# Performance work log

Measured on AMD Instinct MI355X. Metric: run time of the kernel, lower is better.

## Reference

```python
import jax, jax.numpy as jnp
import numpy as np

K = 3            # opt.kernel_size
L = 2            # opt.map_layers
MARGIN = 0.1     # opt.global_margin
NEG_NUM = 3      # opt.neg_num
FIRST_PAD = (K - 1) * L // 2


def conv2d(x, w, pad):
    return jax.lax.conv_general_dilated(x, w, (1, 1), [(pad, pad), (pad, pad)],
                                        dimension_numbers=('NCHW', 'OIHW', 'NCHW'))


def mask2weight(m, pad):
    ker = jnp.ones((1, 1, K, K), jnp.float32)
    w = conv2d(m.astype(jnp.float32)[None, None], ker, pad)[0, 0]
    return jnp.where(w > 0, 1.0 / jnp.maximum(w, 1.0), 0.0)


def setup_inputs():
    key = jax.random.key(0)
    ks = jax.random.split(key, 10)
    b, c, d, t, Lw = 8, 128, 64, 64, 20
    P = d * t
    v_map = jax.random.normal(ks[0], (b, c, d, t), jnp.float32)
    words = jax.random.normal(ks[1], (b, Lw, c), jnp.float32)
    w_masks = jnp.ones((b, Lw), jnp.float32)
    v_mask = jnp.triu(jnp.ones((d, t), jnp.float32))
    valid_num = jax.random.randint(ks[2], (b,), d // 2, t + 1)
    iou_maps = jax.random.uniform(ks[3], (P, P), jnp.float32)
    lam = jnp.float32(0.5)
    sc = np.float32(1.0 / np.sqrt(c * K * K))
    sp = np.float32(1.0 / np.sqrt(c))
    Wc0 = jax.random.normal(ks[4], (c, c, K, K), jnp.float32) * sc
    Wc1 = jax.random.normal(ks[5], (c, c, K, K), jnp.float32) * sc
    bc0 = jnp.zeros((c,), jnp.float32)
    bc1 = jnp.zeros((c,), jnp.float32)
    Wp0 = jax.random.normal(ks[6], (c, c), jnp.float32) * sp
    bp0 = jnp.zeros((c,), jnp.float32)
    Wp1 = jax.random.normal(ks[7], (c, c), jnp.float32) * sp
    bp1 = jnp.zeros((c,), jnp.float32)
    W2d = jax.random.normal(ks[8], (1, c, 1, 1), jnp.float32) * sp
    b2d = jnp.zeros((1,), jnp.float32)
    return dict(v_map=v_map, words=words, w_masks=w_masks, v_mask=v_mask,
                valid_num=valid_num, iou_maps=iou_maps, lam=lam,
                Wc0=Wc0, bc0=bc0, Wc1=Wc1, bc1=bc1,
                Wp0=Wp0, bp0=bp0, Wp1=Wp1, bp1=bp1, W2d=W2d, b2d=b2d)


def _forward(v_map, words, w_masks, v_mask, valid_num, iou_maps, lam,
             Wc0, bc0, Wc1, bc1, Wp0, bp0, Wp1, bp1, W2d, b2d):
    b, c, d, t = v_map.shape
    P = d * t
    neg_inf = jnp.float32(-jnp.inf)
    # mask-normalized conv weights, recomputed from v_mask as in __init__
    weight0 = mask2weight(v_mask, FIRST_PAD)          # [d+2*FIRST_PAD-K+1, ...]
    weight1 = mask2weight(weight0 > 0, 0)             # back to [d, t]
    cols = jnp.arange(t)
    vm3 = (v_mask[None] > 0) & (cols[None, None, :] < valid_num[:, None, None])  # [b,d,t]

    def per_sentence(i):
        wm = w_masks[i]
        pooled = (words[i] * wm[:, None]).sum(0) / jnp.maximum(wm.sum(), 1.0)  # [c]
        g0 = jnp.tanh(pooled @ Wp0 + bp0)
        g1 = jnp.tanh(pooled @ Wp1 + bp1)
        # layer 1 (padded), layer 2 (unpadded) -- word-gated, mask-normalized convs
        x = conv2d(v_map, Wc0, FIRST_PAD) + bc0[None, :, None, None]
        x = jax.nn.relu(x * weight0[None, None] * g0[None, :, None, None])
        x = conv2d(x, Wc1, 0) + bc1[None, :, None, None]
        x = jax.nn.relu(x * weight1[None, None] * g1[None, :, None, None])
        s = jax.nn.sigmoid(conv2d(x, W2d, 0)[:, 0] + b2d[0])  # [b, d, t]
        s = jnp.where(vm3, s, neg_inf)
        pmap_i = s[i]
        sflat = s.reshape(b, P)
        pos = sflat.max(1)          # per-video score for sentence i -> [b]
        si = sflat[i]
        pos_idx = jnp.argmax(si)
        iou_row = iou_maps[pos_idx]  # IoU of best proposal vs all proposals
        negs = jnp.where((iou_row < lam) & jnp.isfinite(si), si, neg_inf)
        hard = negs.max()           # hardest NMS-suppressed negative proposal
        neg_loss = jax.nn.relu(MARGIN + hard - pos[i])
        return pos, pmap_i, neg_loss

    scores, positive_map, neg_losses = jax.lax.map(per_sentence, jnp.arange(b))
    negative_loss = neg_losses.mean()
    diagonal = jnp.diag(scores)[:, None]
    cost_s = jax.nn.relu(MARGIN + scores - diagonal)      # sentence -> video
    cost_im = jax.nn.relu(MARGIN + scores - diagonal.T)   # video -> sentence
    eye = jnp.eye(b, dtype=bool)
    cost_s = jnp.where(eye, 0.0, cost_s)
    cost_im = jnp.where(eye, 0.0, cost_im)
    # max_violation: keep NEG_NUM hardest negatives (sort desc == top_k)
    cost_s = jax.lax.top_k(cost_s, NEG_NUM)[0]
    cost_im = jax.lax.top_k(cost_im.T, NEG_NUM)[0]
    loss = cost_s.sum() / b + cost_im.sum() / b + negative_loss
    return loss, positive_map


def reference(v_map, words, w_masks, v_mask, valid_num, iou_maps, lam,
              Wc0, bc0, Wc1, bc1, Wp0, bp0, Wp1, bp1, W2d, b2d):
    return _forward(v_map, words, w_masks, v_mask, valid_num, iou_maps, lam,
                    Wc0, bc0, Wc1, bc1, Wp0, bp0, Wp1, bp1, W2d, b2d)
```

## Files before the change

kernel.cpp:

```cpp
#include <hip/hip_runtime.h>
#include <hip/hip_bf16.h>
#include <math.h>

#define BB 8
#define CC 128
#define DD 64
#define TT 64
#define PP 4096
#define H1 66
#define LW 20
#define MARGINF 0.1f
#define NEG_SENTINEL -1.0e30f

#define Y0_OFF   0
#define VT_OFF   2230272
#define BP0_OFF  4327424
#define NL_OFF   4401152
#define W0_OFF   4479236
#define W1_OFF   4483592
#define G0_OFF   4487688
#define G1_OFF   4488712
#define S_OFF    4489736
#define SCP_OFF  4522504
#define BP1S_OFF 4522632

typedef __attribute__((ext_vector_type(8))) short bf16x8;
typedef __attribute__((ext_vector_type(4))) float f32x4;

#define ASTR 44

__device__ __forceinline__ unsigned f2bf(float f) {
  union { float f; unsigned u; } v; v.f = f;
  unsigned r = v.u + 0x7fffu + ((v.u >> 16) & 1u);
  return r >> 16;
}
__device__ __forceinline__ float bf2f(unsigned hw) {
  union { unsigned u; float f; } v; v.u = hw << 16;
  return v.f;
}
__device__ __forceinline__ unsigned cvt_bf(float x) {
  __hip_bfloat16 h = __float2bfloat16(x);
  union { __hip_bfloat16 h; unsigned short u; } cv; cv.h = h;
  return (unsigned)cv.u;
}

__device__ __forceinline__ unsigned selbf(unsigned d, unsigned W) {
  unsigned diff = (d ^ W) & 0x80008000u;
  unsigned full = (diff >> 15) * 0xFFFFu;
  return d & ~full;
}

__global__ __launch_bounds__(256) void gates_kernel(
    const float* __restrict__ words, const float* __restrict__ w_masks,
    const float* __restrict__ Wp0, const float* __restrict__ bp0,
    const float* __restrict__ Wp1, const float* __restrict__ bp1,
    float* __restrict__ ws)
{
  __shared__ float smem[CC];
  int i = blockIdx.x;
  int t = threadIdx.x;
  if (t < CC) {
    float wsum = 0.f, acc = 0.f;
    for (int l = 0; l < LW; ++l) {
      float wm = w_masks[i * LW + l];
      wsum += wm;
      acc += words[(i * LW + l) * CC + t] * wm;
    }
    smem[t] = acc / fmaxf(wsum, 1.f);
  }
  __syncthreads();
  {
    int c = t & 127;
    const float* Wp = (t < 128) ? Wp0 : Wp1;
    const float* bp = (t < 128) ? bp0 : bp1;
    float a = bp[c];
    for (int k = 0; k < CC; ++k) a += smem[k] * Wp[k * CC + c];
    float g = tanhf(a);
    float* gout = ws + ((t < 128) ? G0_OFF : G1_OFF);
    gout[i * CC + c] = g;
  }
}

__global__ __launch_bounds__(256) void setup_kernel(
    const float* __restrict__ vmap, const float* __restrict__ v_mask,
    const float* __restrict__ Wc0, const float* __restrict__ Wc1,
    float* __restrict__ ws)
{
  __shared__ float smem[64 * 129];
  int bid = blockIdx.x;
  int t = threadIdx.x;

  if (bid < 576) {
    unsigned short* dst = (unsigned short*)(ws + BP0_OFF);
    int idx = bid * 256 + t;
    int j    = idx & 7;
    int lane = (idx >> 3) & 63;
    int cog  = (idx >> 9) & 7;
    int cic  = (idx >> 12) & 3;
    int kk   = idx >> 14;
    int co = cog * 16 + (lane & 15);
    int ci = cic * 32 + (lane >> 4) * 8 + j;
    dst[idx] = (unsigned short)f2bf(Wc0[(co * CC + ci) * 9 + kk]);
  } else if (bid < 1152) {
    for (int v = t; v < 8 * CC; v += 256) smem[v] = ws[G0_OFF + v];
    __syncthreads();
    int idx = (bid - 576) * 256 + t;
    int j    = idx & 7;
    int lane = (idx >> 3) & 63;
    int cog  = (idx >> 9) & 7;
    int cic  = (idx >> 12) & 3;
    int kk   = idx >> 14;
    int co = cog * 16 + (lane & 15);
    int ci = cic * 32 + (lane >> 4) * 8 + j;
    float wv = Wc1[(co * CC + ci) * 9 + kk];
    unsigned short* dst = (unsigned short*)(ws + BP1S_OFF);
#pragma unroll
    for (int si = 0; si < 8; ++si)
      dst[si * 147456 + idx] = (unsigned short)f2bf(wv * smem[si * CC + ci]);
  } else if (bid < 1664) {
    unsigned short* vT = (unsigned short*)(ws + VT_OFF);
    int b = bid - 1152;
    int n = b & 7, y = b >> 3;
    int x = t & 63, c4 = t >> 6;
    for (int rep = 0; rep < 32; ++rep) {
      int ci = rep * 4 + c4;
      smem[x * 129 + ci] = vmap[(((size_t)n * CC + ci) * DD + y) * TT + x];
    }
    __syncthreads();
    for (int rep = 0; rep < 16; ++rep) {
      int v = t + rep * 256;
      int xx = v >> 6, cip = v & 63;
      float a = smem[xx * 129 + cip * 2];
      float b2 = smem[xx * 129 + cip * 2 + 1];
      unsigned pk = f2bf(a) | (f2bf(b2) << 16);
      *(unsigned*)&vT[(((size_t)(n * DD + y) * TT + xx)) * CC + cip * 2] = pk;
    }
  } else {
    if (t < 128) ((unsigned*)(ws + SCP_OFF))[t] = 0u;
    float* w0 = ws + W0_OFF;
    float* w1 = ws + W1_OFF;
    for (int idx = t; idx < H1 * H1; idx += 256) {
      int y = idx / H1, x = idx % H1;
      float cnt = 0.f;
      for (int ky = 0; ky < 3; ++ky)
        for (int kx = 0; kx < 3; ++kx) {
          int iy = y + ky - 2, ix = x + kx - 2;
          if (iy >= 0 && iy < DD && ix >= 0 && ix < TT) cnt += v_mask[iy * TT + ix];
        }
      w0[idx] = (cnt > 0.f) ? 1.f / fmaxf(cnt, 1.f) : 0.f;
    }
    __syncthreads();
    for (int idx = t; idx < DD * TT; idx += 256) {
      int y = idx / TT, x = idx % TT;
      float cnt = 0.f;
      for (int ky = 0; ky < 3; ++ky)
        for (int kx = 0; kx < 3; ++kx)
          cnt += (w0[(y + ky) * H1 + (x + kx)] > 0.f) ? 1.f : 0.f;
      w1[idx] = (cnt > 0.f) ? 1.f / fmaxf(cnt, 1.f) : 0.f;
    }
  }
}

__global__ __launch_bounds__(256, 2) void conv1_mfma(
    const float* __restrict__ bc0, float* __restrict__ ws)
{
  const unsigned short* vT = (const unsigned short*)(ws + VT_OFF);
  const unsigned short* Bp = (const unsigned short*)(ws + BP0_OFF);
  const float* w0arr = ws + W0_OFF;
  unsigned short* y0w = (unsigned short*)(ws + Y0_OFF);

  __shared__ unsigned short Alds[3 * 68 * ASTR];

  int t = threadIdx.x;
  int id = blockIdx.x + 66 * blockIdx.y;
  int n  = id & 7;
  int r0 = id >> 3;
  int lane = t & 63, w = t >> 6;
  int l15 = lane & 15, l4 = lane >> 4;
  int co0 = w * 32;

  f32x4 acc[5][2];
#pragma unroll
  for (int mf = 0; mf < 5; ++mf)
#pragma unroll
    for (int nf = 0; nf < 2; ++nf) acc[mf][nf] = (f32x4){0.f, 0.f, 0.f, 0.f};

  for (int cic = 0; cic < 4; ++cic) {
    __syncthreads();
    for (int u = t; u < 816; u += 256) {
      int cig = u & 3, rest = u >> 2;
      int col = rest % 68, r = rest / 68;
      int iy = r0 - 2 + r, ix = col - 2;
      uint4 val = {0u, 0u, 0u, 0u};
      if (iy >= 0 && iy < DD && ix >= 0 && ix < TT)
        val = *(const uint4*)&vT[(((size_t)(n * DD + iy) * TT + ix)) * CC + cic * 32 + cig * 8];
      *(uint4*)&Alds[(r * 68 + col) * ASTR + cig * 8] = val;
    }
    __syncthreads();
    __builtin_amdgcn_s_setprio(1);
#pragma unroll
    for (int kk = 0; kk < 9; ++kk) {
      int ky = kk / 3, kx = kk % 3;
      bf16x8 af[5], bfr[2];
#pragma unroll
      for (int mf = 0; mf < 5; ++mf) {
        int c = mf * 16 + l15;
        int cc = c > 65 ? 65 : c;
        af[mf] = *(const bf16x8*)&Alds[(ky * 68 + cc + kx) * ASTR + l4 * 8];
      }
#pragma unroll
      for (int nf = 0; nf < 2; ++nf)
        bfr[nf] = *(const bf16x8*)&Bp[(((kk * 4 + cic) * 8 + w * 2 + nf) * 64 + lane) * 8];
#pragma unroll
      for (int mf = 0; mf < 5; ++mf)
#pragma unroll
        for (int nf = 0; nf < 2; ++nf)
          acc[mf][nf] = __builtin_amdgcn_mfma_f32_16x16x32_bf16(af[mf], bfr[nf], acc[mf][nf], 0, 0, 0);
    }
    __builtin_amdgcn_s_setprio(0);
  }

  int y = r0;
#pragma unroll
  for (int nf = 0; nf < 2; ++nf) {
    int co = co0 + nf * 16 + l15;
    float bcv = bc0[co];
#pragma unroll
    for (int mf = 0; mf < 5; ++mf)
#pragma unroll
      for (int rg = 0; rg < 4; ++rg) {
        int c = mf * 16 + l4 * 4 + rg;
        if (c < H1) {
          float v = (acc[mf][nf][rg] + bcv) * w0arr[y * H1 + c];
          y0w[((size_t)(n * H1 + y) * H1 + c) * CC + co] = (unsigned short)cvt_bf(v);
        }
      }
  }
}

__global__ __launch_bounds__(256, 3) void conv2_mfma(
    const float* __restrict__ bc1, const float* __restrict__ W2d,
    const float* __restrict__ b2d, const float* __restrict__ v_mask,
    const int* __restrict__ valid_num, float* __restrict__ ws,
    float* __restrict__ out)
{
  const unsigned short* y0w = (const unsigned short*)(ws + Y0_OFF);
  const float* w1m = ws + W1_OFF;
  const float* g0 = ws + G0_OFF;
  const float* g1 = ws + G1_OFF;
  unsigned long long* scp = (unsigned long long*)(ws + SCP_OFF);

  __shared__ unsigned short Alds[4 * 66 * ASTR];
  __shared__ unsigned msk[16][4];
  __shared__ float redl[2][2][64];
  __shared__ unsigned long long kred[2];

  int t = threadIdx.x;
  int r0 = blockIdx.x;
  int i = blockIdx.y & 7, n = blockIdx.y >> 3;
  int lane = t & 63, w = t >> 6;
  int wr = w >> 1, wc = w & 1;
  int l15 = lane & 15, l4 = lane >> 4;

  const unsigned short* Bp = (const unsigned short*)(ws + BP1S_OFF) + (size_t)i * 147456;

  if (t < 16) {
    int ch = t * 8;
    msk[t][0] = (g0[i * CC + ch + 0] > 0.f ? 0u : 0x8000u) | (g0[i * CC + ch + 1] > 0.f ? 0u : 0x80000000u);
    msk[t][1] = (g0[i * CC + ch + 2] > 0.f ? 0u : 0x8000u) | (g0[i * CC + ch + 3] > 0.f ? 0u : 0x80000000u);
    msk[t][2] = (g0[i * CC + ch + 4] > 0.f ? 0u : 0x8000u) | (g0[i * CC + ch + 5] > 0.f ? 0u : 0x80000000u);
    msk[t][3] = (g0[i * CC + ch + 6] > 0.f ? 0u : 0x8000u) | (g0[i * CC + ch + 7] > 0.f ? 0u : 0x80000000u);
  }

  f32x4 acc[4][4];
#pragma unroll
  for (int mf = 0; mf < 4; ++mf)
#pragma unroll
    for (int nf = 0; nf < 4; ++nf) acc[mf][nf] = (f32x4){0.f, 0.f, 0.f, 0.f};

  for (int cic = 0; cic < 4; ++cic) {
    __syncthreads();
    {
      uint4 mv = *(const uint4*)&msk[(cic << 2) | (t & 3)][0];
      for (int u = t; u < 1056; u += 256) {
        int cig = u & 3, cr = u >> 2;
        int col = cr % 66, row = cr / 66;
        const unsigned short* src = y0w
            + ((size_t)((n * H1 + r0 * 2 + row) * H1 + col)) * CC + cic * 32 + cig * 8;
        uint4 raw = *(const uint4*)src;
        uint4 pk;
        pk.x = selbf(raw.x, mv.x);
        pk.y = selbf(raw.y, mv.y);
        pk.z = selbf(raw.z, mv.z);
        pk.w = selbf(raw.w, mv.w);
        *(uint4*)&Alds[(row * 66 + col) * ASTR + cig * 8] = pk;
      }
    }
    __syncthreads();
    __builtin_amdgcn_s_setprio(1);
#pragma unroll
    for (int kk = 0; kk < 9; ++kk) {
      int ky = kk / 3, kx = kk % 3;
      bf16x8 af[4], bfr[4];
#pragma unroll
      for (int mf = 0; mf < 4; ++mf) {
        int row = wr + ky;
        int col = mf * 16 + l15 + kx;
        af[mf] = *(const bf16x8*)&Alds[(row * 66 + col) * ASTR + l4 * 8];
      }
#pragma unroll
      for (int nf = 0; nf < 4; ++nf)
        bfr[nf] = *(const bf16x8*)&Bp[(((kk * 4 + cic) * 8 + wc * 4 + nf) * 64 + lane) * 8];
#pragma unroll
      for (int mf = 0; mf < 4; ++mf)
#pragma unroll
        for (int nf = 0; nf < 4; ++nf)
          acc[mf][nf] = __builtin_amdgcn_mfma_f32_16x16x32_bf16(af[mf], bfr[nf], acc[mf][nf], 0, 0, 0);
    }
    __builtin_amdgcn_s_setprio(0);
  }

  float part[4][4];
#pragma unroll
  for (int mf = 0; mf < 4; ++mf)
#pragma unroll
    for (int rg = 0; rg < 4; ++rg) part[mf][rg] = 0.f;
#pragma unroll
  for (int nf = 0; nf < 4; ++nf) {
    int co = wc * 64 + nf * 16 + l15;
    float bcv = bc1[co];
    float gv = g1[i * CC + co];
    float wv = W2d[co];
#pragma unroll
    for (int mf = 0; mf < 4; ++mf)
#pragma unroll
      for (int rg = 0; rg < 4; ++rg) {
        float z = (acc[mf][nf][rg] + bcv) * gv;
        part[mf][rg] += fmaxf(z, 0.f) * wv;
      }
  }
#pragma unroll
  for (int mask = 1; mask < 16; mask <<= 1)
#pragma unroll
    for (int mf = 0; mf < 4; ++mf)
#pragma unroll
      for (int rg = 0; rg < 4; ++rg)
        part[mf][rg] += __shfl_xor(part[mf][rg], mask, 64);
  if (l15 == 0) {
#pragma unroll
    for (int mf = 0; mf < 4; ++mf)
#pragma unroll
      for (int rg = 0; rg < 4; ++rg)
        redl[wc][wr][mf * 16 + l4 * 4 + rg] = part[mf][rg];
  }
  __syncthreads();
  if (t < 128) {
    int row = t >> 6, col = t & 63;
    int rowg = r0 * 2 + row;
    float v = redl[0][row][col] + redl[1][row][col];
    float logit = w1m[rowg * TT + col] * v + b2d[0];
    float sig = 1.f / (1.f + expf(-logit));
    bool m = (v_mask[rowg * TT + col] > 0.f) && (col < valid_num[n]);
    int p = rowg * TT + col;
    if (i == n) {
      ws[S_OFF + i * PP + p] = m ? sig : -INFINITY;
      out[1 + i * PP + p] = m ? sig : NEG_SENTINEL;
    }
    unsigned long long key = 0ull;
    if (m) key = ((unsigned long long)__float_as_uint(sig) << 32)
                 | (unsigned long long)(0xFFFFFFFFu - (unsigned)p);
#pragma unroll
    for (int mk = 1; mk < 64; mk <<= 1) {
      unsigned lo = __shfl_xor((unsigned)key, mk, 64);
      unsigned hi = __shfl_xor((unsigned)(key >> 32), mk, 64);
      unsigned long long o = ((unsigned long long)hi << 32) | lo;
      if (o > key) key = o;
    }
    if (lane == 0) kred[w] = key;
  }
  __syncthreads();
  if (t == 0) {
    unsigned long long k = kred[0];
    if (kred[1] > k) k = kred[1];
    if (k) atomicMax(&scp[i * 8 + n], k);
  }
}

__global__ __launch_bounds__(256) void mine_kernel(
    const float* __restrict__ iou_maps, const float* __restrict__ lam,
    float* __restrict__ ws)
{
  __shared__ float wred[4];
  int i = blockIdx.x;
  int t = threadIdx.x, lane = t & 63, w = t >> 6;
  const unsigned long long* scp = (const unsigned long long*)(ws + SCP_OFF);

  unsigned long long dk = scp[i * 9];
  float diag_sc = __uint_as_float((unsigned)(dk >> 32));
  int pidx = (int)(0xFFFFFFFFu - (unsigned)(dk & 0xFFFFFFFFu));
  float lamv = lam[0];
  const float* row = iou_maps + (size_t)pidx * PP;
  const float* si = ws + S_OFF + (size_t)i * PP;
  float hv = -INFINITY;
  for (int p = t; p < PP; p += 256) {
    float v = si[p];
    if (row[p] < lamv && isfinite(v)) hv = fmaxf(hv, v);
  }
#pragma unroll
  for (int m = 1; m < 64; m <<= 1) hv = fmaxf(hv, __shfl_xor(hv, m, 64));
  if (lane == 0) wred[w] = hv;
  __syncthreads();
  if (t == 0) {
    float h = fmaxf(fmaxf(wred[0], wred[1]), fmaxf(wred[2], wred[3]));
    ws[NL_OFF + i] = fmaxf(0.f, MARGINF + h - diag_sc);
  }
}

__global__ __launch_bounds__(64) void loss_kernel(
    float* __restrict__ ws, float* __restrict__ out)
{
  __shared__ float scsh[64];
  int lane = threadIdx.x;
  const unsigned long long* scp = (const unsigned long long*)(ws + SCP_OFF);
  scsh[lane] = __uint_as_float((unsigned)(scp[lane] >> 32));
  __syncthreads();

  float partial = 0.f;
  if (lane < 16) {
    int r = lane & 7;
    bool im = lane >= 8;
    float diag = scsh[r * 8 + r];
    float v[8];
#pragma unroll
    for (int j = 0; j < 8; ++j) {
      float scv = im ? scsh[j * 8 + r] : scsh[r * 8 + j];
      float h = fmaxf(0.f, MARGINF + scv - diag);
      v[j] = (j == r) ? 0.f : h;
    }
#define CE(a, b) { float mx = fmaxf(v[a], v[b]); float mn = fminf(v[a], v[b]); v[a] = mx; v[b] = mn; }
    CE(0,1) CE(2,3) CE(4,5) CE(6,7)
    CE(0,2) CE(1,3) CE(4,6) CE(5,7)
    CE(1,2) CE(5,6)
    CE(0,4) CE(1,5) CE(2,6) CE(3,7)
    CE(2,4) CE(3,5)
    CE(1,2) CE(3,4) CE(5,6)
#undef CE
    partial = v[0] + v[1] + v[2];
  } else if (lane >= 16 && lane < 24) {
    partial = ws[NL_OFF + lane - 16];
  }
#pragma unroll
  for (int m = 1; m < 64; m <<= 1) partial += __shfl_xor(partial, m, 64);
  if (lane == 0) out[0] = partial * 0.125f;
}

extern "C" void kernel_launch(void* const* d_in, const int* in_sizes, int n_in,
                              void* d_out, int out_size, void* d_ws, size_t ws_size,
                              hipStream_t stream)
{
  const float* v_map     = (const float*)d_in[0];
  const float* words     = (const float*)d_in[1];
  const float* w_masks   = (const float*)d_in[2];
  const float* v_mask    = (const float*)d_in[3];
  const int*   valid_num = (const int*)d_in[4];
  const float* iou_maps  = (const float*)d_in[5];
  const float* lam       = (const float*)d_in[6];
  const float* Wc0 = (const float*)d_in[7];
  const float* bc0 = (const float*)d_in[8];
  const float* Wc1 = (const float*)d_in[9];
  const float* bc1 = (const float*)d_in[10];
  const float* Wp0 = (const float*)d_in[11];
  const float* bp0 = (const float*)d_in[12];
  const float* Wp1 = (const float*)d_in[13];
  const float* bp1 = (const float*)d_in[14];
  const float* W2d = (const float*)d_in[15];
  const float* b2d = (const float*)d_in[16];
  float* ws  = (float*)d_ws;
  float* out = (float*)d_out;

  hipLaunchKernelGGL(gates_kernel, dim3(8), dim3(256), 0, stream,
                     words, w_masks, Wp0, bp0, Wp1, bp1, ws);
  hipLaunchKernelGGL(setup_kernel, dim3(1665), dim3(256), 0, stream,
                     v_map, v_mask, Wc0, Wc1, ws);
  hipLaunchKernelGGL(conv1_mfma, dim3(66, 8), dim3(256), 0, stream, bc0, ws);
  hipLaunchKernelGGL(conv2_mfma, dim3(32, 64), dim3(256), 0, stream,
                     bc1, W2d, b2d, v_mask, valid_num, ws, out);
  hipLaunchKernelGGL(mine_kernel, dim3(8), dim3(256), 0, stream, iou_maps, lam, ws);
  hipLaunchKernelGGL(loss_kernel, dim3(1), dim3(64), 0, stream, ws, out);
}
```

Before: 141.8 us.

## Fuse gates into setup, move Wc1 prep into conv1, split conv1 channels

```diff
diff --git a/kernel.cpp b/kernel.cpp
--- a/kernel.cpp
+++ b/kernel.cpp
@@ -50,40 +50,12 @@
   return d & ~full;
 }
 
-__global__ __launch_bounds__(256) void gates_kernel(
+__global__ __launch_bounds__(256) void setup_kernel(
+    const float* __restrict__ vmap, const float* __restrict__ v_mask,
+    const float* __restrict__ Wc0,
     const float* __restrict__ words, const float* __restrict__ w_masks,
     const float* __restrict__ Wp0, const float* __restrict__ bp0,
     const float* __restrict__ Wp1, const float* __restrict__ bp1,
-    float* __restrict__ ws)
-{
-  __shared__ float smem[CC];
-  int i = blockIdx.x;
-  int t = threadIdx.x;
-  if (t < CC) {
-    float wsum = 0.f, acc = 0.f;
-    for (int l = 0; l < LW; ++l) {
-      float wm = w_masks[i * LW + l];
-      wsum += wm;
-      acc += words[(i * LW + l) * CC + t] * wm;
-    }
-    smem[t] = acc / fmaxf(wsum, 1.f);
-  }
-  __syncthreads();
-  {
-    int c = t & 127;
-    const float* Wp = (t < 128) ? Wp0 : Wp1;
-    const float* bp = (t < 128) ? bp0 : bp1;
-    float a = bp[c];
-    for (int k = 0; k < CC; ++k) a += smem[k] * Wp[k * CC + c];
-    float g = tanhf(a);
-    float* gout = ws + ((t < 128) ? G0_OFF : G1_OFF);
-    gout[i * CC + c] = g;
-  }
-}
-
-__global__ __launch_bounds__(256) void setup_kernel(
-    const float* __restrict__ vmap, const float* __restrict__ v_mask,
-    const float* __restrict__ Wc0, const float* __restrict__ Wc1,
     float* __restrict__ ws)
 {
   __shared__ float smem[64 * 129];
@@ -101,25 +73,9 @@
     int co = cog * 16 + (lane & 15);
     int ci = cic * 32 + (lane >> 4) * 8 + j;
     dst[idx] = (unsigned short)f2bf(Wc0[(co * CC + ci) * 9 + kk]);
-  } else if (bid < 1152) {
-    for (int v = t; v < 8 * CC; v += 256) smem[v] = ws[G0_OFF + v];
-    __syncthreads();
-    int idx = (bid - 576) * 256 + t;
-    int j    = idx & 7;
-    int lane = (idx >> 3) & 63;
-    int cog  = (idx >> 9) & 7;
-    int cic  = (idx >> 12) & 3;
-    int kk   = idx >> 14;
-    int co = cog * 16 + (lane & 15);
-    int ci = cic * 32 + (lane >> 4) * 8 + j;
-    float wv = Wc1[(co * CC + ci) * 9 + kk];
-    unsigned short* dst = (unsigned short*)(ws + BP1S_OFF);
-#pragma unroll
-    for (int si = 0; si < 8; ++si)
-      dst[si * 147456 + idx] = (unsigned short)f2bf(wv * smem[si * CC + ci]);
-  } else if (bid < 1664) {
+  } else if (bid < 1088) {
     unsigned short* vT = (unsigned short*)(ws + VT_OFF);
-    int b = bid - 1152;
+    int b = bid - 576;
     int n = b & 7, y = b >> 3;
     int x = t & 63, c4 = t >> 6;
     for (int rep = 0; rep < 32; ++rep) {
@@ -135,7 +91,7 @@
       unsigned pk = f2bf(a) | (f2bf(b2) << 16);
       *(unsigned*)&vT[(((size_t)(n * DD + y) * TT + xx)) * CC + cip * 2] = pk;
     }
-  } else {
+  } else if (bid == 1088) {
     if (t < 128) ((unsigned*)(ws + SCP_OFF))[t] = 0u;
     float* w0 = ws + W0_OFF;
     float* w1 = ws + W1_OFF;
@@ -158,32 +114,76 @@
           cnt += (w0[(y + ky) * H1 + (x + kx)] > 0.f) ? 1.f : 0.f;
       w1[idx] = (cnt > 0.f) ? 1.f / fmaxf(cnt, 1.f) : 0.f;
     }
-  }
-}
-
-__global__ __launch_bounds__(256, 2) void conv1_mfma(
-    const float* __restrict__ bc0, float* __restrict__ ws)
-{
+  } else {
+    int i = bid - 1089;
+    if (t < CC) {
+      float wsum = 0.f, acc = 0.f;
+      for (int l = 0; l < LW; ++l) {
+        float wm = w_masks[i * LW + l];
+        wsum += wm;
+        acc += words[(i * LW + l) * CC + t] * wm;
+      }
+      smem[t] = acc / fmaxf(wsum, 1.f);
+    }
+    __syncthreads();
+    {
+      int c = t & 127;
+      const float* Wp = (t < 128) ? Wp0 : Wp1;
+      const float* bp = (t < 128) ? bp0 : bp1;
+      float a = bp[c];
+      for (int k = 0; k < CC; ++k) a += smem[k] * Wp[k * CC + c];
+      float g = tanhf(a);
+      float* gout = ws + ((t < 128) ? G0_OFF : G1_OFF);
+      gout[i * CC + c] = g;
+    }
+  }
+}
+
+__global__ __launch_bounds__(256, 3) void conv1_mfma(
+    const float* __restrict__ bc0, const float* __restrict__ Wc1,
+    float* __restrict__ ws)
+{
+  __shared__ unsigned short Alds[3 * 68 * ASTR];
+
+  int t = threadIdx.x;
+  int id = blockIdx.x;
+
+  if (id >= 1056) {
+    float* smem = (float*)Alds;
+    for (int v = t; v < 8 * CC; v += 256) smem[v] = ws[G0_OFF + v];
+    __syncthreads();
+    int idx = (id - 1056) * 256 + t;
+    int j    = idx & 7;
+    int lane = (idx >> 3) & 63;
+    int cog  = (idx >> 9) & 7;
+    int cic  = (idx >> 12) & 3;
+    int kk   = idx >> 14;
+    int co = cog * 16 + (lane & 15);
+    int ci = cic * 32 + (lane >> 4) * 8 + j;
+    float wv = Wc1[(co * CC + ci) * 9 + kk];
+    unsigned short* dst = (unsigned short*)(ws + BP1S_OFF);
+#pragma unroll
+    for (int si = 0; si < 8; ++si)
+      dst[si * 147456 + idx] = (unsigned short)f2bf(wv * smem[si * CC + ci]);
+    return;
+  }
+
   const unsigned short* vT = (const unsigned short*)(ws + VT_OFF);
   const unsigned short* Bp = (const unsigned short*)(ws + BP0_OFF);
   const float* w0arr = ws + W0_OFF;
   unsigned short* y0w = (unsigned short*)(ws + Y0_OFF);
 
-  __shared__ unsigned short Alds[3 * 68 * ASTR];
-
-  int t = threadIdx.x;
-  int id = blockIdx.x + 66 * blockIdx.y;
   int n  = id & 7;
-  int r0 = id >> 3;
+  int ch = (id >> 3) & 1;
+  int r0 = id >> 4;
   int lane = t & 63, w = t >> 6;
   int l15 = lane & 15, l4 = lane >> 4;
-  int co0 = w * 32;
-
-  f32x4 acc[5][2];
-#pragma unroll
-  for (int mf = 0; mf < 5; ++mf)
-#pragma unroll
-    for (int nf = 0; nf < 2; ++nf) acc[mf][nf] = (f32x4){0.f, 0.f, 0.f, 0.f};
+  int s = ch * 4 + w;
+  int co0 = s * 16;
+
+  f32x4 acc[5];
+#pragma unroll
+  for (int mf = 0; mf < 5; ++mf) acc[mf] = (f32x4){0.f, 0.f, 0.f, 0.f};
 
   for (int cic = 0; cic < 4; ++cic) {
     __syncthreads();
@@ -201,29 +201,24 @@
 #pragma unroll
     for (int kk = 0; kk < 9; ++kk) {
       int ky = kk / 3, kx = kk % 3;
-      bf16x8 af[5], bfr[2];
+      bf16x8 af[5], bfr;
 #pragma unroll
       for (int mf = 0; mf < 5; ++mf) {
         int c = mf * 16 + l15;
         int cc = c > 65 ? 65 : c;
         af[mf] = *(const bf16x8*)&Alds[(ky * 68 + cc + kx) * ASTR + l4 * 8];
       }
-#pragma unroll
-      for (int nf = 0; nf < 2; ++nf)
-        bfr[nf] = *(const bf16x8*)&Bp[(((kk * 4 + cic) * 8 + w * 2 + nf) * 64 + lane) * 8];
+      bfr = *(const bf16x8*)&Bp[(((kk * 4 + cic) * 8 + s) * 64 + lane) * 8];
 #pragma unroll
       for (int mf = 0; mf < 5; ++mf)
-#pragma unroll
-        for (int nf = 0; nf < 2; ++nf)
-          acc[mf][nf] = __builtin_amdgcn_mfma_f32_16x16x32_bf16(af[mf], bfr[nf], acc[mf][nf], 0, 0, 0);
+        acc[mf] = __builtin_amdgcn_mfma_f32_16x16x32_bf16(af[mf], bfr, acc[mf], 0, 0, 0);
     }
     __builtin_amdgcn_s_setprio(0);
   }
 
   int y = r0;
-#pragma unroll
-  for (int nf = 0; nf < 2; ++nf) {
-    int co = co0 + nf * 16 + l15;
+  {
+    int co = co0 + l15;
     float bcv = bc0[co];
 #pragma unroll
     for (int mf = 0; mf < 5; ++mf)
@@ -231,7 +226,7 @@
       for (int rg = 0; rg < 4; ++rg) {
         int c = mf * 16 + l4 * 4 + rg;
         if (c < H1) {
-          float v = (acc[mf][nf][rg] + bcv) * w0arr[y * H1 + c];
+          float v = (acc[mf][rg] + bcv) * w0arr[y * H1 + c];
           y0w[((size_t)(n * H1 + y) * H1 + c) * CC + co] = (unsigned short)cvt_bf(v);
         }
       }
@@ -478,11 +473,9 @@
   float* ws  = (float*)d_ws;
   float* out = (float*)d_out;
 
-  hipLaunchKernelGGL(gates_kernel, dim3(8), dim3(256), 0, stream,
-                     words, w_masks, Wp0, bp0, Wp1, bp1, ws);
-  hipLaunchKernelGGL(setup_kernel, dim3(1665), dim3(256), 0, stream,
-                     v_map, v_mask, Wc0, Wc1, ws);
-  hipLaunchKernelGGL(conv1_mfma, dim3(66, 8), dim3(256), 0, stream, bc0, ws);
+  hipLaunchKernelGGL(setup_kernel, dim3(1097), dim3(256), 0, stream,
+                     v_map, v_mask, Wc0, words, w_masks, Wp0, bp0, Wp1, bp1, ws);
+  hipLaunchKernelGGL(conv1_mfma, dim3(1632), dim3(256), 0, stream, bc0, Wc1, ws);
   hipLaunchKernelGGL(conv2_mfma, dim3(32, 64), dim3(256), 0, stream,
                      bc1, W2d, b2d, v_mask, valid_num, ws, out);
   hipLaunchKernelGGL(mine_kernel, dim3(8), dim3(256), 0, stream, iou_maps, lam, ws);
```

Result: faster. 133.8 us (median of 4 runs) (-5.6%).
